# Kernel optimization log

Hardware: AMD Instinct MI355X
Metric: run time of the kernel (lower is better)

## Reference

```python
import jax, jax.numpy as jnp
import numpy as np

N_ATOMS = 50000
N_EDGES = 1_600_000
H = 128
EPS = 1e-3  # keras BatchNormalization default epsilon


def _bn(x, gamma, beta, mean, var):
    # inference-mode batch norm with moving statistics
    return gamma * (x - mean) * jax.lax.rsqrt(var + EPS) + beta


def setup_inputs() -> dict:
    key = jax.random.key(0)
    ks = jax.random.split(key, 16)
    s = 0.05
    D1 = H + 1
    inp = {
        "atom_embedding": jax.random.normal(ks[0], (N_ATOMS, H), jnp.float32),
        "bond_embedding": jax.random.normal(ks[1], (N_EDGES, H), jnp.float32),
        "indices_i": jax.random.randint(ks[2], (N_EDGES,), 0, N_ATOMS, dtype=jnp.int32),
        "indices_j": jax.random.randint(ks[3], (N_EDGES,), 0, N_ATOMS, dtype=jnp.int32),
        # preprocess: Dense(3H -> H+1, no bias) + BN, Dense(H+1 -> H+1, no bias) + BN
        "W1": jax.random.normal(ks[4], (3 * H, D1), jnp.float32) * s,
        "g1": jnp.ones((D1,), jnp.float32),
        "b1": jnp.zeros((D1,), jnp.float32),
        "m1": jnp.zeros((D1,), jnp.float32),
        "v1": jnp.ones((D1,), jnp.float32),
        "W2": jax.random.normal(ks[5], (D1, D1), jnp.float32) * s,
        "g2": jnp.ones((D1,), jnp.float32),
        "b2": jnp.zeros((D1,), jnp.float32),
        "m2": jnp.zeros((D1,), jnp.float32),
        "v2": jnp.ones((D1,), jnp.float32),
        # two residual layers, each: x + (x@w1+b1)@w2+b2 (activation=None)
        "r1w1": jax.random.normal(ks[6], (H, H), jnp.float32) * s,
        "r1b1": jnp.zeros((H,), jnp.float32),
        "r1w2": jax.random.normal(ks[7], (H, H), jnp.float32) * s,
        "r1b2": jnp.zeros((H,), jnp.float32),
        "r2w1": jax.random.normal(ks[8], (H, H), jnp.float32) * s,
        "r2b1": jnp.zeros((H,), jnp.float32),
        "r2w2": jax.random.normal(ks[9], (H, H), jnp.float32) * s,
        "r2b2": jnp.zeros((H,), jnp.float32),
    }
    return inp


def reference(atom_embedding, bond_embedding, indices_i, indices_j,
              W1, g1, b1, m1, v1, W2, g2, b2, m2, v2,
              r1w1, r1b1, r1w2, r1b2, r2w1, r2b1, r2w2, r2b2):
    # gather endpoints: [E, H]
    ai = atom_embedding[indices_i]
    aj = atom_embedding[indices_j]
    x = jnp.concatenate([ai, bond_embedding, aj], axis=-1)  # [E, 3H]
    x = _bn(x @ W1, g1, b1, m1, v1)  # [E, H+1]
    x = _bn(x @ W2, g2, b2, m2, v2)  # [E, H+1]
    msg = x[:, :1] * x[:, 1:]  # gate * message -> [E, H]
    atom = atom_embedding + jax.ops.segment_sum(msg, indices_i, num_segments=N_ATOMS)
    # residual MLPs (activation=None -> identity)
    atom = atom + (atom @ r1w1 + r1b1) @ r1w2 + r1b2
    atom = atom + (atom @ r2w1 + r2b1) @ r2w2 + r2b2
    return atom
```

## Files before the change

kernel.cpp:

```cpp
#include <hip/hip_runtime.h>

#define NA 50000
#define NE 1600000
#define HH 128
#define D1 129
#define EPS 1e-3f

typedef __bf16 bf16_t;
typedef bf16_t bf16x8 __attribute__((ext_vector_type(8)));
typedef bf16_t bf16x4 __attribute__((ext_vector_type(4)));
typedef float f32x4 __attribute__((ext_vector_type(4)));

#define OFF_A1   0
#define OFF_C1   129
#define OFF_A2   258
#define OFF_C2   387
#define OFF_WEFF 516
#define OFF_DVEC (OFF_WEFF + 384*129)
#define OFF_Q1   (OFF_DVEC + 129)
#define OFF_Q2   (OFF_Q1 + 128*128)
#define OFF_q1   (OFF_Q2 + 128*128)
#define OFF_q2   (OFF_q1 + 128)
#define OFF_QF   (OFF_q2 + 128)
#define OFF_qf   (OFF_QF + 128*128)
#define OFF_WMT  (((OFF_qf + 128) + 3) & ~3)
#define OFF_WTT  (OFF_WMT + 9216)
#define OFF_WBT  (OFF_WTT + 9216)
#define OFF_QFT  (OFF_WBT + 9216)
#define OFF_PI   (OFF_QFT + 8192)
#define OFF_PJ   (OFF_PI + NA*D1)
#define OFF_ACC  (OFF_PJ + NA*D1)
#define OFF_ACC2 (OFF_ACC + NA*HH)
#define OFF_CNT  (OFF_ACC2 + NA)
#define OFF_CUR  (OFF_CNT + NA)
#define OFF_EDG  (OFF_CUR + NA)
#define OFF_PART (OFF_EDG + NE)
#define SCAN_NB  ((NA + 255) / 256)

__global__ void k_affine(const float* __restrict__ g1, const float* __restrict__ b1,
                         const float* __restrict__ m1, const float* __restrict__ v1,
                         const float* __restrict__ g2, const float* __restrict__ b2,
                         const float* __restrict__ m2, const float* __restrict__ v2,
                         float* __restrict__ ws) {
    for (int idx = threadIdx.x; idx < 2 * D1; idx += blockDim.x) {
        if (idx < D1) {
            float a = g1[idx] * rsqrtf(v1[idx] + EPS);
            ws[OFF_A1 + idx] = a;
            ws[OFF_C1 + idx] = b1[idx] - m1[idx] * a;
        } else {
            int n = idx - D1;
            float a = g2[n] * rsqrtf(v2[n] + EPS);
            ws[OFF_A2 + n] = a;
            ws[OFF_C2 + n] = b2[n] - m2[n] * a;
        }
    }
}

__global__ void k_weff(const float* __restrict__ W1, const float* __restrict__ W2,
                       float* __restrict__ ws) {
    int idx = blockIdx.x * blockDim.x + threadIdx.x;
    if (idx >= 384 * D1 + D1) return;
    const float* a1 = ws + OFF_A1;
    const float* c1 = ws + OFF_C1;
    const float* a2 = ws + OFF_A2;
    const float* c2 = ws + OFF_C2;
    if (idx < 384 * D1) {
        int k = idx / D1, n = idx % D1;
        float s = 0.f;
        for (int t = 0; t < D1; ++t)
            s += W1[(size_t)k * D1 + t] * a1[t] * W2[(size_t)t * D1 + n];
        ws[OFF_WEFF + idx] = s * a2[n];
    } else {
        int n = idx - 384 * D1;
        float s = 0.f;
        for (int t = 0; t < D1; ++t)
            s += c1[t] * W2[(size_t)t * D1 + n];
        ws[OFF_DVEC + n] = s * a2[n] + c2[n];
    }
}

__global__ void k_resid(const float* __restrict__ r1w1, const float* __restrict__ r1b1,
                        const float* __restrict__ r1w2, const float* __restrict__ r1b2,
                        const float* __restrict__ r2w1, const float* __restrict__ r2b1,
                        const float* __restrict__ r2w2, const float* __restrict__ r2b2,
                        float* __restrict__ ws) {
    int idx = blockIdx.x * blockDim.x + threadIdx.x;
    if (idx >= 2 * (128 * 128 + 128)) return;
    int layer = idx / (128 * 128 + 128);
    int r = idx % (128 * 128 + 128);
    const float* w1 = layer ? r2w1 : r1w1;
    const float* b1 = layer ? r2b1 : r1b1;
    const float* w2 = layer ? r2w2 : r1w2;
    const float* b2 = layer ? r2b2 : r1b2;
    float* Q = ws + (layer ? OFF_Q2 : OFF_Q1);
    float* q = ws + (layer ? OFF_q2 : OFF_q1);
    if (r < 128 * 128) {
        int i = r >> 7, j = r & 127;
        float s = (i == j) ? 1.f : 0.f;
        for (int t = 0; t < 128; ++t)
            s += w1[i * 128 + t] * w2[t * 128 + j];
        Q[r] = s;
    } else {
        int j = r - 128 * 128;
        float s = b2[j];
        for (int t = 0; t < 128; ++t)
            s += b1[t] * w2[t * 128 + j];
        q[j] = s;
    }
}

__global__ void k_qf(float* __restrict__ ws) {
    int idx = blockIdx.x * blockDim.x + threadIdx.x;
    if (idx >= 128 * 128 + 128) return;
    const float* Q1 = ws + OFF_Q1;
    const float* Q2 = ws + OFF_Q2;
    if (idx < 128 * 128) {
        int i = idx >> 7, j = idx & 127;
        float s = 0.f;
        for (int m = 0; m < 128; ++m)
            s += Q1[i * 128 + m] * Q2[m * 128 + j];
        ws[OFF_QF + idx] = s;
    } else {
        int j = idx - 128 * 128;
        const float* q1 = ws + OFF_q1;
        float s = ws[OFF_q2 + j];
        for (int m = 0; m < 128; ++m)
            s += q1[m] * Q2[m * 128 + j];
        ws[OFF_qf + j] = s;
    }
}

__global__ void k_pack(float* __restrict__ ws) {
    int idx = blockIdx.x * blockDim.x + threadIdx.x;
    const float* Weff = ws + OFF_WEFF;
    if (idx < 18432) {
        int n = idx >> 7, k = idx & 127;
        float v = (n < 128) ? Weff[(size_t)(128 + k) * D1 + n + 1]
                            : ((n == 128) ? Weff[(size_t)(128 + k) * D1] : 0.f);
        ((bf16_t*)(ws + OFF_WMT))[idx] = (bf16_t)v;
    } else if (idx < 2 * 18432) {
        int r = idx - 18432;
        int n = r >> 7, k = r & 127;
        float v = (n < D1) ? Weff[(size_t)k * D1 + n] : 0.f;
        ((bf16_t*)(ws + OFF_WTT))[r] = (bf16_t)v;
    } else if (idx < 3 * 18432) {
        int r = idx - 2 * 18432;
        int n = r >> 7, k = r & 127;
        float v = (n < D1) ? Weff[(size_t)(256 + k) * D1 + n] : 0.f;
        ((bf16_t*)(ws + OFF_WBT))[r] = (bf16_t)v;
    } else if (idx < 3 * 18432 + 16384) {
        int r = idx - 3 * 18432;
        int n = r >> 7, k = r & 127;
        ((bf16_t*)(ws + OFF_QFT))[r] = (bf16_t)ws[OFF_QF + k * 128 + n];
    }
}

__global__ void k_hist(const int* __restrict__ idx_i, float* __restrict__ ws) {
    int e = blockIdx.x * blockDim.x + threadIdx.x;
    if (e < NE) atomicAdd((int*)(ws + OFF_CNT) + idx_i[e], 1);
}

__global__ void k_scan1(float* __restrict__ ws) {
    const int* cnt = (const int*)(ws + OFF_CNT);
    int i = blockIdx.x * 256 + threadIdx.x;
    int v = (i < NA) ? cnt[i] : 0;
#pragma unroll
    for (int o = 1; o < 64; o <<= 1) v += __shfl_xor(v, o);
    __shared__ int wsum[4];
    if ((threadIdx.x & 63) == 0) wsum[threadIdx.x >> 6] = v;
    __syncthreads();
    if (threadIdx.x == 0)
        ((int*)(ws + OFF_PART))[blockIdx.x] = wsum[0] + wsum[1] + wsum[2] + wsum[3];
}

__global__ void k_scan2(float* __restrict__ ws) {
    int* part = (int*)(ws + OFF_PART);
    __shared__ int ps[256];
    int t = threadIdx.x;
    int v = (t < SCAN_NB) ? part[t] : 0;
    ps[t] = v;
    __syncthreads();
    for (int o = 1; o < 256; o <<= 1) {
        int u = (t >= o) ? ps[t - o] : 0;
        __syncthreads();
        ps[t] += u;
        __syncthreads();
    }
    part[t] = t ? ps[t - 1] : 0;
}

__global__ void k_scan3(float* __restrict__ ws) {
    const int* cnt = (const int*)(ws + OFF_CNT);
    int* cursor = (int*)(ws + OFF_CUR);
    int base = ((const int*)(ws + OFF_PART))[blockIdx.x];
    int i = blockIdx.x * 256 + threadIdx.x;
    int v = (i < NA) ? cnt[i] : 0;
    int lane = threadIdx.x & 63, w = threadIdx.x >> 6;
    int s = v;
#pragma unroll
    for (int o = 1; o < 64; o <<= 1) {
        int u = __shfl_up(s, o);
        if (lane >= o) s += u;
    }
    __shared__ int wtot[4];
    if (lane == 63) wtot[w] = s;
    __syncthreads();
    int add = 0;
    for (int k = 0; k < 4; ++k)
        if (k < w) add += wtot[k];
    if (i < NA) cursor[i] = base + add + s - v;
}

__global__ void k_scatter(const int* __restrict__ idx_i, float* __restrict__ ws) {
    int e = blockIdx.x * blockDim.x + threadIdx.x;
    if (e < NE) {
        int i = idx_i[e];
        int p = atomicAdd((int*)(ws + OFF_CUR) + i, 1);
        ((int*)(ws + OFF_EDG))[p] = e;
    }
}

__global__ __launch_bounds__(256) void k_gemm_mfma(
    const float* __restrict__ A, const float* __restrict__ A2,
    const float* __restrict__ Pi, const float* __restrict__ acc2,
    const bf16_t* __restrict__ Wt, const float* __restrict__ bias,
    float* __restrict__ C, int ldc, int N, int ntiles, int M) {
    __shared__ __align__(16) bf16_t As[64][136];
    int t = threadIdx.x;
    int m0 = blockIdx.x * 64;
#pragma unroll
    for (int it = 0; it < 8; ++it) {
        int idx = t + 256 * it;
        int r = idx >> 5, c4 = idx & 31;
        int grow = m0 + r;
        float4 v = make_float4(0.f, 0.f, 0.f, 0.f);
        if (grow < M) {
            v = ((const float4*)(A + (size_t)grow * 128))[c4];
            if (A2) {
                float4 w = ((const float4*)(A2 + (size_t)grow * 128))[c4];
                v.x += w.x; v.y += w.y; v.z += w.z; v.w += w.w;
            }
            if (acc2) {
                float s = acc2[grow];
                const float* p = Pi + (size_t)grow * D1 + 1 + c4 * 4;
                v.x += s * p[0]; v.y += s * p[1]; v.z += s * p[2]; v.w += s * p[3];
            }
        }
        bf16x4 tmp;
        tmp[0] = (bf16_t)v.x; tmp[1] = (bf16_t)v.y; tmp[2] = (bf16_t)v.z; tmp[3] = (bf16_t)v.w;
        *(bf16x4*)&As[r][c4 * 4] = tmp;
    }
    __syncthreads();
    int lane = t & 63, w = t >> 6;
    int ll = lane & 15, quad = lane >> 4;
    bf16x8 a[4];
#pragma unroll
    for (int k = 0; k < 4; ++k)
        a[k] = *(const bf16x8*)&As[w * 16 + ll][k * 32 + quad * 8];
    for (int nt = 0; nt < ntiles; ++nt) {
        const bf16_t* bp = Wt + (size_t)(nt * 16 + ll) * 128 + quad * 8;
        f32x4 acc = {0.f, 0.f, 0.f, 0.f};
#pragma unroll
        for (int k = 0; k < 4; ++k) {
            bf16x8 b = *(const bf16x8*)(bp + k * 32);
            acc = __builtin_amdgcn_mfma_f32_16x16x32_bf16(a[k], b, acc, 0, 0, 0);
        }
        int col = nt * 16 + ll;
        if (col < N) {
            float bv = bias ? bias[col] : 0.f;
#pragma unroll
            for (int r = 0; r < 4; ++r) {
                int row = m0 + w * 16 + quad * 4 + r;
                if (row < M) C[(size_t)row * ldc + col] = acc[r] + bv;
            }
        }
    }
}

__global__ __launch_bounds__(256) void k_pipj(
    const float* __restrict__ A, const bf16_t* __restrict__ Wt,
    const float* __restrict__ bias, float* __restrict__ Ct,
    const bf16_t* __restrict__ Wb, float* __restrict__ Cb, int M) {
    __shared__ __align__(16) bf16_t As[64][136];
    int t = threadIdx.x;
    int m0 = blockIdx.x * 64;
#pragma unroll
    for (int it = 0; it < 8; ++it) {
        int idx = t + 256 * it;
        int r = idx >> 5, c4 = idx & 31;
        int grow = m0 + r;
        float4 v = make_float4(0.f, 0.f, 0.f, 0.f);
        if (grow < M) v = ((const float4*)(A + (size_t)grow * 128))[c4];
        bf16x4 tmp;
        tmp[0] = (bf16_t)v.x; tmp[1] = (bf16_t)v.y; tmp[2] = (bf16_t)v.z; tmp[3] = (bf16_t)v.w;
        *(bf16x4*)&As[r][c4 * 4] = tmp;
    }
    __syncthreads();
    int lane = t & 63, w = t >> 6;
    int ll = lane & 15, quad = lane >> 4;
    bf16x8 a[4];
#pragma unroll
    for (int k = 0; k < 4; ++k)
        a[k] = *(const bf16x8*)&As[w * 16 + ll][k * 32 + quad * 8];
    for (int half = 0; half < 2; ++half) {
        const bf16_t* W = half ? Wb : Wt;
        float* C = half ? Cb : Ct;
        for (int nt = 0; nt < 9; ++nt) {
            const bf16_t* bp = W + (size_t)(nt * 16 + ll) * 128 + quad * 8;
            f32x4 acc = {0.f, 0.f, 0.f, 0.f};
#pragma unroll
            for (int k = 0; k < 4; ++k) {
                bf16x8 b = *(const bf16x8*)(bp + k * 32);
                acc = __builtin_amdgcn_mfma_f32_16x16x32_bf16(a[k], b, acc, 0, 0, 0);
            }
            int col = nt * 16 + ll;
            if (col < D1) {
                float bv = (half == 0 && bias) ? bias[col] : 0.f;
#pragma unroll
                for (int r = 0; r < 4; ++r) {
                    int row = m0 + w * 16 + quad * 4 + r;
                    if (row < M) C[(size_t)row * D1 + col] = acc[r] + bv;
                }
            }
        }
    }
}

__global__ __launch_bounds__(256) void k_edge_mfma(
    const float* __restrict__ bond, const int* __restrict__ idx_i,
    const int* __restrict__ idx_j, const int* __restrict__ edge_of,
    const bf16_t* __restrict__ WmidT,
    const float* __restrict__ Pi, const float* __restrict__ Pj,
    float* __restrict__ accb, float* __restrict__ acc2) {
    int t = threadIdx.x;
    int lane = t & 63, w = t >> 6;
    int ll = lane & 15, quad = lane >> 4;
    size_t p0 = (size_t)blockIdx.x * 256;

    bf16x8 bg[4], bn0[4], bn1[4];
    {
        const bf16_t* gp = WmidT + (size_t)(128 + ll) * 128 + quad * 8;
        const bf16_t* q0 = WmidT + (size_t)((w * 2) * 16 + ll) * 128 + quad * 8;
        const bf16_t* q1 = WmidT + (size_t)((w * 2 + 1) * 16 + ll) * 128 + quad * 8;
#pragma unroll
        for (int k = 0; k < 4; ++k) {
            bg[k] = *(const bf16x8*)(gp + k * 32);
            bn0[k] = *(const bf16x8*)(q0 + k * 32);
            bn1[k] = *(const bf16x8*)(q1 + k * 32);
        }
    }
    int n0 = (w * 2) * 16 + ll, n1 = (w * 2 + 1) * 16 + ll;

    for (int g = 0; g < 16; ++g) {
        int base = g * 16;
        int e = edge_of[p0 + base + ll];
        int iv = idx_i[e], jv = idx_j[e];
        int ipv = __shfl(iv, (ll + 15) & 15);
        unsigned bmask = (unsigned)(__ballot(ll > 0 && iv != ipv) & 0xFFFFu);
        int jr[4], ir[4];
#pragma unroll
        for (int r = 0; r < 4; ++r) {
            jr[r] = __shfl(jv, quad * 4 + r);
            ir[r] = __shfl(iv, quad * 4 + r);
        }

        const float4* brow = (const float4*)(bond + (size_t)e * 128);
        bf16x8 a[4];
#pragma unroll
        for (int k = 0; k < 4; ++k) {
            float4 u = brow[k * 8 + quad * 2];
            float4 v = brow[k * 8 + quad * 2 + 1];
            bf16x8 tmp;
            tmp[0] = (bf16_t)u.x; tmp[1] = (bf16_t)u.y;
            tmp[2] = (bf16_t)u.z; tmp[3] = (bf16_t)u.w;
            tmp[4] = (bf16_t)v.x; tmp[5] = (bf16_t)v.y;
            tmp[6] = (bf16_t)v.z; tmp[7] = (bf16_t)v.w;
            a[k] = tmp;
        }

        f32x4 ag = {0.f, 0.f, 0.f, 0.f};
#pragma unroll
        for (int k = 0; k < 4; ++k)
            ag = __builtin_amdgcn_mfma_f32_16x16x32_bf16(a[k], bg[k], ag, 0, 0, 0);
        float gl[4];
#pragma unroll
        for (int r = 0; r < 4; ++r) {
            float v = ag[r];
            if (ll == 0) v += Pi[(size_t)ir[r] * D1] + Pj[(size_t)jr[r] * D1];
            gl[r] = __shfl(v, lane & 48);
        }

        if (w == 0) {
            int rs = 0;
            while (rs < 16) {
                unsigned rest = bmask >> (rs + 1);
                int re = rest ? rs + 1 + __builtin_ctz(rest) : 16;
                float s = 0.f;
#pragma unroll
                for (int r = 0; r < 4; ++r) {
                    int ee = quad * 4 + r;
                    if (ee >= rs && ee < re) s += gl[r];
                }
                s += __shfl_xor(s, 16);
                s += __shfl_xor(s, 32);
                int irs = __shfl(iv, rs);
                if (lane == 0) atomicAdd(&acc2[irs], s);
                rs = re;
            }
        }

        float pj0[4], pj1[4];
#pragma unroll
        for (int r = 0; r < 4; ++r) {
            const float* pjr = Pj + (size_t)jr[r] * D1 + 1;
            pj0[r] = pjr[n0];
            pj1[r] = pjr[n1];
        }
        f32x4 ac0 = {0.f, 0.f, 0.f, 0.f}, ac1 = {0.f, 0.f, 0.f, 0.f};
#pragma unroll
        for (int k = 0; k < 4; ++k)
            ac0 = __builtin_amdgcn_mfma_f32_16x16x32_bf16(a[k], bn0[k], ac0, 0, 0, 0);
#pragma unroll
        for (int k = 0; k < 4; ++k)
            ac1 = __builtin_amdgcn_mfma_f32_16x16x32_bf16(a[k], bn1[k], ac1, 0, 0, 0);
        float m0[4], m1[4];
#pragma unroll
        for (int r = 0; r < 4; ++r) {
            m0[r] = gl[r] * (ac0[r] + pj0[r]);
            m1[r] = gl[r] * (ac1[r] + pj1[r]);
        }

        {
            int rs = 0;
            while (rs < 16) {
                unsigned rest = bmask >> (rs + 1);
                int re = rest ? rs + 1 + __builtin_ctz(rest) : 16;
                float s0 = 0.f, s1 = 0.f;
#pragma unroll
                for (int r = 0; r < 4; ++r) {
                    int ee = quad * 4 + r;
                    if (ee >= rs && ee < re) { s0 += m0[r]; s1 += m1[r]; }
                }
                s0 += __shfl_xor(s0, 16);
                s0 += __shfl_xor(s0, 32);
                s1 += __shfl_xor(s1, 16);
                s1 += __shfl_xor(s1, 32);
                int irs = __shfl(iv, rs);
                if (quad == 0) {
                    float* ab = accb + (size_t)irs * 128;
                    atomicAdd(ab + n0, s0);
                    atomicAdd(ab + n1, s1);
                }
                rs = re;
            }
        }
    }
}

extern "C" void kernel_launch(void* const* d_in, const int* in_sizes, int n_in,
                              void* d_out, int out_size, void* d_ws, size_t ws_size,
                              hipStream_t stream) {
    const float* atom = (const float*)d_in[0];
    const float* bond = (const float*)d_in[1];
    const int* idx_i = (const int*)d_in[2];
    const int* idx_j = (const int*)d_in[3];
    const float* W1 = (const float*)d_in[4];
    const float* g1 = (const float*)d_in[5];
    const float* b1 = (const float*)d_in[6];
    const float* m1 = (const float*)d_in[7];
    const float* v1 = (const float*)d_in[8];
    const float* W2 = (const float*)d_in[9];
    const float* g2 = (const float*)d_in[10];
    const float* b2 = (const float*)d_in[11];
    const float* m2 = (const float*)d_in[12];
    const float* v2 = (const float*)d_in[13];
    const float* r1w1 = (const float*)d_in[14];
    const float* r1b1 = (const float*)d_in[15];
    const float* r1w2 = (const float*)d_in[16];
    const float* r1b2 = (const float*)d_in[17];
    const float* r2w1 = (const float*)d_in[18];
    const float* r2b1 = (const float*)d_in[19];
    const float* r2w2 = (const float*)d_in[20];
    const float* r2b2 = (const float*)d_in[21];
    float* ws = (float*)d_ws;
    float* out = (float*)d_out;

    hipMemsetAsync(ws + OFF_ACC, 0, (size_t)(NA * HH + 2 * NA) * sizeof(float), stream);

    k_hist<<<(NE + 255) / 256, 256, 0, stream>>>(idx_i, ws);
    k_scan1<<<SCAN_NB, 256, 0, stream>>>(ws);
    k_scan2<<<1, 256, 0, stream>>>(ws);
    k_scan3<<<SCAN_NB, 256, 0, stream>>>(ws);
    k_scatter<<<(NE + 255) / 256, 256, 0, stream>>>(idx_i, ws);

    k_affine<<<1, 256, 0, stream>>>(g1, b1, m1, v1, g2, b2, m2, v2, ws);
    k_weff<<<(384 * D1 + D1 + 255) / 256, 256, 0, stream>>>(W1, W2, ws);
    k_resid<<<(2 * (128 * 128 + 128) + 255) / 256, 256, 0, stream>>>(
        r1w1, r1b1, r1w2, r1b2, r2w1, r2b1, r2w2, r2b2, ws);
    k_qf<<<(128 * 128 + 128 + 255) / 256, 256, 0, stream>>>(ws);
    k_pack<<<(3 * 18432 + 16384 + 255) / 256, 256, 0, stream>>>(ws);

    int gblocks = (NA + 63) / 64;
    k_pipj<<<gblocks, 256, 0, stream>>>(
        atom, (const bf16_t*)(ws + OFF_WTT), ws + OFF_DVEC, ws + OFF_PI,
        (const bf16_t*)(ws + OFF_WBT), ws + OFF_PJ, NA);

    k_edge_mfma<<<NE / 256, 256, 0, stream>>>(
        bond, idx_i, idx_j, (const int*)(ws + OFF_EDG), (const bf16_t*)(ws + OFF_WMT),
        ws + OFF_PI, ws + OFF_PJ, ws + OFF_ACC, ws + OFF_ACC2);

    k_gemm_mfma<<<gblocks, 256, 0, stream>>>(
        atom, ws + OFF_ACC, ws + OFF_PI, ws + OFF_ACC2, (const bf16_t*)(ws + OFF_QFT),
        ws + OFF_qf, out, 128, 128, 8, NA);
}
```

Measured before the change: 1.915 ms.

## Stage bond rows through double-buffered LDS and pre-sort edge indices

The edge kernel now loads 64 bond rows per tile cooperatively with coalesced float4 loads into a double-buffered LDS tile, converting them to bf16. The next tile is prefetched into registers while MFMA work runs on the current one. The scatter kernel writes the i/j indices in sorted order, so the edge kernel no longer does dependent gathers of idx_i and idx_j through edge_of. Adds about 35KB of LDS per block, a per-tile barrier and an occupancy hint of 3 blocks, which may limit occupancy. The scatter also does more writes.

```diff
diff --git a/kernel.cpp b/kernel.cpp
--- a/kernel.cpp
+++ b/kernel.cpp
@@ -35,6 +35,8 @@
 #define OFF_CUR  (OFF_CNT + NA)
 #define OFF_EDG  (OFF_CUR + NA)
 #define OFF_PART (OFF_EDG + NE)
+#define OFF_IIS  (OFF_PART + 256)
+#define OFF_JJS  (OFF_IIS + NE)
 #define SCAN_NB  ((NA + 255) / 256)
 
 __global__ void k_affine(const float* __restrict__ g1, const float* __restrict__ b1,
@@ -211,12 +213,15 @@
     if (i < NA) cursor[i] = base + add + s - v;
 }
 
-__global__ void k_scatter(const int* __restrict__ idx_i, float* __restrict__ ws) {
+__global__ void k_scatter(const int* __restrict__ idx_i, const int* __restrict__ idx_j,
+                          float* __restrict__ ws) {
     int e = blockIdx.x * blockDim.x + threadIdx.x;
     if (e < NE) {
         int i = idx_i[e];
         int p = atomicAdd((int*)(ws + OFF_CUR) + i, 1);
         ((int*)(ws + OFF_EDG))[p] = e;
+        ((int*)(ws + OFF_IIS))[p] = i;
+        ((int*)(ws + OFF_JJS))[p] = idx_j[e];
     }
 }
 
@@ -326,12 +331,15 @@
     }
 }
 
-__global__ __launch_bounds__(256) void k_edge_mfma(
-    const float* __restrict__ bond, const int* __restrict__ idx_i,
-    const int* __restrict__ idx_j, const int* __restrict__ edge_of,
+__global__ __launch_bounds__(256, 3) void k_edge_mfma(
+    const float* __restrict__ bond, const int* __restrict__ edge_of,
+    const int* __restrict__ ii_srt, const int* __restrict__ jj_srt,
     const bf16_t* __restrict__ WmidT,
     const float* __restrict__ Pi, const float* __restrict__ Pj,
     float* __restrict__ accb, float* __restrict__ acc2) {
+    __shared__ __align__(16) bf16_t As[2][64][136];
+    __shared__ int ii2[2][64], jj2[2][64];
+
     int t = threadIdx.x;
     int lane = t & 63, w = t >> 6;
     int ll = lane & 15, quad = lane >> 4;
@@ -340,8 +348,8 @@
     bf16x8 bg[4], bn0[4], bn1[4];
     {
         const bf16_t* gp = WmidT + (size_t)(128 + ll) * 128 + quad * 8;
-        const bf16_t* q0 = WmidT + (size_t)((w * 2) * 16 + ll) * 128 + quad * 8;
-        const bf16_t* q1 = WmidT + (size_t)((w * 2 + 1) * 16 + ll) * 128 + quad * 8;
+        const bf16_t* q0 = WmidT + (size_t)(w * 32 + ll) * 128 + quad * 8;
+        const bf16_t* q1 = WmidT + (size_t)(w * 32 + 16 + ll) * 128 + quad * 8;
 #pragma unroll
         for (int k = 0; k < 4; ++k) {
             bg[k] = *(const bf16x8*)(gp + k * 32);
@@ -349,88 +357,111 @@
             bn1[k] = *(const bf16x8*)(q1 + k * 32);
         }
     }
-    int n0 = (w * 2) * 16 + ll, n1 = (w * 2 + 1) * 16 + ll;
-
-    for (int g = 0; g < 16; ++g) {
-        int base = g * 16;
-        int e = edge_of[p0 + base + ll];
-        int iv = idx_i[e], jv = idx_j[e];
-        int ipv = __shfl(iv, (ll + 15) & 15);
-        unsigned bmask = (unsigned)(__ballot(ll > 0 && iv != ipv) & 0xFFFFu);
-        int jr[4], ir[4];
-#pragma unroll
-        for (int r = 0; r < 4; ++r) {
-            jr[r] = __shfl(jv, quad * 4 + r);
-            ir[r] = __shfl(iv, quad * 4 + r);
-        }
-
-        const float4* brow = (const float4*)(bond + (size_t)e * 128);
-        bf16x8 a[4];
-#pragma unroll
-        for (int k = 0; k < 4; ++k) {
-            float4 u = brow[k * 8 + quad * 2];
-            float4 v = brow[k * 8 + quad * 2 + 1];
-            bf16x8 tmp;
-            tmp[0] = (bf16_t)u.x; tmp[1] = (bf16_t)u.y;
-            tmp[2] = (bf16_t)u.z; tmp[3] = (bf16_t)u.w;
-            tmp[4] = (bf16_t)v.x; tmp[5] = (bf16_t)v.y;
-            tmp[6] = (bf16_t)v.z; tmp[7] = (bf16_t)v.w;
-            a[k] = tmp;
-        }
-
-        f32x4 ag = {0.f, 0.f, 0.f, 0.f};
-#pragma unroll
-        for (int k = 0; k < 4; ++k)
-            ag = __builtin_amdgcn_mfma_f32_16x16x32_bf16(a[k], bg[k], ag, 0, 0, 0);
-        float gl[4];
-#pragma unroll
-        for (int r = 0; r < 4; ++r) {
-            float v = ag[r];
-            if (ll == 0) v += Pi[(size_t)ir[r] * D1] + Pj[(size_t)jr[r] * D1];
-            gl[r] = __shfl(v, lane & 48);
-        }
-
-        if (w == 0) {
-            int rs = 0;
-            while (rs < 16) {
-                unsigned rest = bmask >> (rs + 1);
-                int re = rest ? rs + 1 + __builtin_ctz(rest) : 16;
-                float s = 0.f;
-#pragma unroll
-                for (int r = 0; r < 4; ++r) {
-                    int ee = quad * 4 + r;
-                    if (ee >= rs && ee < re) s += gl[r];
+    int n0 = w * 32 + ll, n1 = w * 32 + 16 + ll;
+
+#pragma unroll
+    for (int it = 0; it < 8; ++it) {
+        int idx = t + 256 * it;
+        int r = idx >> 5, c4 = idx & 31;
+        int e = edge_of[p0 + r];
+        float4 v = ((const float4*)(bond + (size_t)e * 128))[c4];
+        bf16x4 tmp;
+        tmp[0] = (bf16_t)v.x; tmp[1] = (bf16_t)v.y; tmp[2] = (bf16_t)v.z; tmp[3] = (bf16_t)v.w;
+        *(bf16x4*)&As[0][r][c4 * 4] = tmp;
+    }
+    if (t < 64) {
+        ii2[0][t] = ii_srt[p0 + t];
+        jj2[0][t] = jj_srt[p0 + t];
+    }
+    __syncthreads();
+
+    for (int tt = 0; tt < 4; ++tt) {
+        int buf = tt & 1;
+
+        float4 pf[8];
+        int ni = 0, nj = 0;
+        if (tt < 3) {
+            size_t nb = p0 + (size_t)(tt + 1) * 64;
+#pragma unroll
+            for (int it = 0; it < 8; ++it) {
+                int idx = t + 256 * it;
+                int r = idx >> 5, c4 = idx & 31;
+                int e = edge_of[nb + r];
+                pf[it] = ((const float4*)(bond + (size_t)e * 128))[c4];
+            }
+            if (t < 64) {
+                ni = ii_srt[nb + t];
+                nj = jj_srt[nb + t];
+            }
+        }
+
+#pragma unroll
+        for (int g = 0; g < 4; ++g) {
+            int eb = g * 16;
+            bf16x8 a[4];
+#pragma unroll
+            for (int k = 0; k < 4; ++k)
+                a[k] = *(const bf16x8*)&As[buf][eb + ll][k * 32 + quad * 8];
+
+            int my = ii2[buf][eb + ll];
+            int pv = ll ? ii2[buf][eb + ll - 1] : my;
+            unsigned bmask = (unsigned)(__ballot(lane < 16 && my != pv) & 0xFFFFull);
+
+            f32x4 ag = {0.f, 0.f, 0.f, 0.f};
+#pragma unroll
+            for (int k = 0; k < 4; ++k)
+                ag = __builtin_amdgcn_mfma_f32_16x16x32_bf16(a[k], bg[k], ag, 0, 0, 0);
+            float gl[4];
+#pragma unroll
+            for (int r = 0; r < 4; ++r) {
+                float v = ag[r];
+                if (ll == 0) {
+                    int ie = ii2[buf][eb + quad * 4 + r];
+                    int je = jj2[buf][eb + quad * 4 + r];
+                    v += Pi[(size_t)ie * D1] + Pj[(size_t)je * D1];
                 }
-                s += __shfl_xor(s, 16);
-                s += __shfl_xor(s, 32);
-                int irs = __shfl(iv, rs);
-                if (lane == 0) atomicAdd(&acc2[irs], s);
-                rs = re;
-            }
-        }
-
-        float pj0[4], pj1[4];
-#pragma unroll
-        for (int r = 0; r < 4; ++r) {
-            const float* pjr = Pj + (size_t)jr[r] * D1 + 1;
-            pj0[r] = pjr[n0];
-            pj1[r] = pjr[n1];
-        }
-        f32x4 ac0 = {0.f, 0.f, 0.f, 0.f}, ac1 = {0.f, 0.f, 0.f, 0.f};
-#pragma unroll
-        for (int k = 0; k < 4; ++k)
-            ac0 = __builtin_amdgcn_mfma_f32_16x16x32_bf16(a[k], bn0[k], ac0, 0, 0, 0);
-#pragma unroll
-        for (int k = 0; k < 4; ++k)
-            ac1 = __builtin_amdgcn_mfma_f32_16x16x32_bf16(a[k], bn1[k], ac1, 0, 0, 0);
-        float m0[4], m1[4];
-#pragma unroll
-        for (int r = 0; r < 4; ++r) {
-            m0[r] = gl[r] * (ac0[r] + pj0[r]);
-            m1[r] = gl[r] * (ac1[r] + pj1[r]);
-        }
-
-        {
+                gl[r] = __shfl(v, lane & 48);
+            }
+
+            if (w == 0) {
+                int rs = 0;
+                while (rs < 16) {
+                    unsigned rest = bmask >> (rs + 1);
+                    int re = rest ? rs + 1 + __builtin_ctz(rest) : 16;
+                    float s = 0.f;
+#pragma unroll
+                    for (int r = 0; r < 4; ++r) {
+                        int ee = quad * 4 + r;
+                        if (ee >= rs && ee < re) s += gl[r];
+                    }
+                    s += __shfl_xor(s, 16);
+                    s += __shfl_xor(s, 32);
+                    if (lane == 0) atomicAdd(&acc2[ii2[buf][eb + rs]], s);
+                    rs = re;
+                }
+            }
+
+            float pj0[4], pj1[4];
+#pragma unroll
+            for (int r = 0; r < 4; ++r) {
+                const float* pjr = Pj + (size_t)jj2[buf][eb + quad * 4 + r] * D1 + 1;
+                pj0[r] = pjr[n0];
+                pj1[r] = pjr[n1];
+            }
+            f32x4 ac0 = {0.f, 0.f, 0.f, 0.f}, ac1 = {0.f, 0.f, 0.f, 0.f};
+#pragma unroll
+            for (int k = 0; k < 4; ++k)
+                ac0 = __builtin_amdgcn_mfma_f32_16x16x32_bf16(a[k], bn0[k], ac0, 0, 0, 0);
+#pragma unroll
+            for (int k = 0; k < 4; ++k)
+                ac1 = __builtin_amdgcn_mfma_f32_16x16x32_bf16(a[k], bn1[k], ac1, 0, 0, 0);
+            float m0[4], m1[4];
+#pragma unroll
+            for (int r = 0; r < 4; ++r) {
+                m0[r] = gl[r] * (ac0[r] + pj0[r]);
+                m1[r] = gl[r] * (ac1[r] + pj1[r]);
+            }
+
             int rs = 0;
             while (rs < 16) {
                 unsigned rest = bmask >> (rs + 1);
@@ -445,15 +476,32 @@
                 s0 += __shfl_xor(s0, 32);
                 s1 += __shfl_xor(s1, 16);
                 s1 += __shfl_xor(s1, 32);
-                int irs = __shfl(iv, rs);
                 if (quad == 0) {
-                    float* ab = accb + (size_t)irs * 128;
+                    float* ab = accb + (size_t)ii2[buf][eb + rs] * 128;
                     atomicAdd(ab + n0, s0);
                     atomicAdd(ab + n1, s1);
                 }
                 rs = re;
             }
         }
+
+        if (tt < 3) {
+            int nbuf = buf ^ 1;
+#pragma unroll
+            for (int it = 0; it < 8; ++it) {
+                int idx = t + 256 * it;
+                int r = idx >> 5, c4 = idx & 31;
+                bf16x4 tmp;
+                tmp[0] = (bf16_t)pf[it].x; tmp[1] = (bf16_t)pf[it].y;
+                tmp[2] = (bf16_t)pf[it].z; tmp[3] = (bf16_t)pf[it].w;
+                *(bf16x4*)&As[nbuf][r][c4 * 4] = tmp;
+            }
+            if (t < 64) {
+                ii2[nbuf][t] = ni;
+                jj2[nbuf][t] = nj;
+            }
+        }
+        __syncthreads();
     }
 }
 
@@ -491,7 +539,7 @@
     k_scan1<<<SCAN_NB, 256, 0, stream>>>(ws);
     k_scan2<<<1, 256, 0, stream>>>(ws);
     k_scan3<<<SCAN_NB, 256, 0, stream>>>(ws);
-    k_scatter<<<(NE + 255) / 256, 256, 0, stream>>>(idx_i, ws);
+    k_scatter<<<(NE + 255) / 256, 256, 0, stream>>>(idx_i, idx_j, ws);
 
     k_affine<<<1, 256, 0, stream>>>(g1, b1, m1, v1, g2, b2, m2, v2, ws);
     k_weff<<<(384 * D1 + D1 + 255) / 256, 256, 0, stream>>>(W1, W2, ws);
@@ -506,7 +554,8 @@
         (const bf16_t*)(ws + OFF_WBT), ws + OFF_PJ, NA);
 
     k_edge_mfma<<<NE / 256, 256, 0, stream>>>(
-        bond, idx_i, idx_j, (const int*)(ws + OFF_EDG), (const bf16_t*)(ws + OFF_WMT),
+        bond, (const int*)(ws + OFF_EDG), (const int*)(ws + OFF_IIS),
+        (const int*)(ws + OFF_JJS), (const bf16_t*)(ws + OFF_WMT),
         ws + OFF_PI, ws + OFF_PJ, ws + OFF_ACC, ws + OFF_ACC2);
 
     k_gemm_mfma<<<gblocks, 256, 0, stream>>>(
```

After: 1.710 ms. 1.12x faster.
